# Kernel optimization log

Hardware: AMD Instinct MI355X
Metric: run time of the kernel (lower is better)

Reference implementation:

```python
import jax, jax.numpy as jnp
import numpy as np

N_NODES = 50000
IN_FEATS, H_FEATS, OUT_FEATS = 128, 128, 40
N_EDGES = 800000


def gcn_conv(x, src, dst, deg_inv_sqrt, W, b):
    # PyG GCNConv (eval): h = x @ W; msg = norm * h[src]; out = scatter_add(msg -> dst) + b
    h = x @ W  # [N, F_out]
    norm = deg_inv_sqrt[src] * deg_inv_sqrt[dst]  # [E+N] (self-loops included)
    msg = h[src] * norm[:, None]
    out = jax.ops.segment_sum(msg, dst, num_segments=x.shape[0])
    return out + b


def setup_inputs() -> dict:
    key = jax.random.key(0)
    k1, k2, k3, k4 = jax.random.split(key, 4)
    x = jax.random.normal(k1, (N_NODES, IN_FEATS), dtype=jnp.float32)
    edge_index = jax.random.randint(k2, (2, N_EDGES), 0, N_NODES, dtype=jnp.int64)
    # Glorot-ish init for weights, zeros for bias (PyG default)
    W1 = jax.random.normal(k3, (IN_FEATS, H_FEATS), dtype=jnp.float32) / np.sqrt(IN_FEATS)
    b1 = jnp.zeros((H_FEATS,), dtype=jnp.float32)
    W2 = jax.random.normal(k4, (H_FEATS, OUT_FEATS), dtype=jnp.float32) / np.sqrt(H_FEATS)
    b2 = jnp.zeros((OUT_FEATS,), dtype=jnp.float32)
    return {"x": x, "edge_index": edge_index, "W1": W1, "b1": b1, "W2": W2, "b2": b2}


def reference(x, edge_index, W1, b1, W2, b2):
    n = x.shape[0]
    loop = jnp.arange(n, dtype=edge_index.dtype)
    src = jnp.concatenate([edge_index[0], loop])  # add self-loops
    dst = jnp.concatenate([edge_index[1], loop])
    # symmetric normalization: deg over destinations (incl. self-loops)
    deg = jnp.zeros((n,), dtype=x.dtype).at[dst].add(1.0)
    deg_inv_sqrt = jnp.where(deg > 0, jax.lax.rsqrt(deg), 0.0)
    # dropout(p=0.6) is identity in eval mode
    h = jax.nn.relu(gcn_conv(x, src, dst, deg_inv_sqrt, W1, b1))
    out = gcn_conv(h, src, dst, deg_inv_sqrt, W2, b2)
    return out
```

## Files before the change

### kernel.cpp

```cpp
#include <hip/hip_runtime.h>
#include <hip/hip_fp16.h>

#define THREADS 256
#define EPB 2048


__global__ __launch_bounds__(256) void k_hist(const int* __restrict__ dst,
                                              int* __restrict__ Hmat,
                                              int e, int nbuck, int nbpad) {
    __shared__ int h[256];
    const int t = threadIdx.x;
    h[t] = 0;
    __syncthreads();
    const int base = blockIdx.x * EPB;
#pragma unroll
    for (int k = 0; k < 8; ++k) {
        int i = base + k * 256 + t;
        if (i < e) atomicAdd(&h[dst[i] >> 8], 1);
    }
    __syncthreads();
    if (t < nbuck) Hmat[t * nbpad + blockIdx.x] = h[t];
}

__global__ __launch_bounds__(256) void k_bscan(const int* __restrict__ Hmat,
                                               int* __restrict__ Off,
                                               int* __restrict__ btot,
                                               int nb, int nbpad) {
    __shared__ int s[256];
    const int b = blockIdx.x, t = threadIdx.x;
    const int* H = Hmat + b * nbpad;
    const int v0 = (2 * t     < nb) ? H[2 * t]     : 0;
    const int v1 = (2 * t + 1 < nb) ? H[2 * t + 1] : 0;
    const int p = v0 + v1;
    s[t] = p;
    __syncthreads();
    for (int off = 1; off < 256; off <<= 1) {
        int w = (t >= off) ? s[t - off] : 0;
        __syncthreads();
        s[t] += w;
        __syncthreads();
    }
    const int excl = s[t] - p;
    int* O = Off + b * nbpad;
    if (2 * t     < nb) O[2 * t]     = excl;
    if (2 * t + 1 < nb) O[2 * t + 1] = excl + v0;
    if (t == 255) btot[b] = s[255];
}

__global__ __launch_bounds__(256) void k_base(const int* __restrict__ btot,
                                              int* __restrict__ bbase,
                                              int* __restrict__ rowptr,
                                              int nbuck, int n, int e) {
    __shared__ int s[256];
    const int t = threadIdx.x;
    const int v = (t < nbuck) ? btot[t] : 0;
    s[t] = v;
    __syncthreads();
    for (int off = 1; off < 256; off <<= 1) {
        int w = (t >= off) ? s[t - off] : 0;
        __syncthreads();
        s[t] += w;
        __syncthreads();
    }
    if (t < nbuck) bbase[t] = s[t] - v;
    if (t == 0) { bbase[nbuck] = e; rowptr[n] = e; }
}

__global__ __launch_bounds__(256) void k_scat(const int* __restrict__ src,
                                              const int* __restrict__ dst,
                                              const int* __restrict__ Off,
                                              const int* __restrict__ bbase,
                                              int2* __restrict__ sorted,
                                              int e, int nbpad) {
    __shared__ int h[256];
    const int t = threadIdx.x;
    h[t] = 0;
    __syncthreads();
    const int base = blockIdx.x * EPB;
#pragma unroll
    for (int k = 0; k < 8; ++k) {
        int i = base + k * 256 + t;
        if (i < e) {
            const int d = dst[i];
            const int b = d >> 8;
            const int r = atomicAdd(&h[b], 1);
            const int pos = bbase[b] + Off[b * nbpad + blockIdx.x] + r;
            sorted[pos] = make_int2(src[i], d);
        }
    }
}

__global__ __launch_bounds__(256) void k_bsort(const int2* __restrict__ sorted,
                                               const int* __restrict__ bbase,
                                               int* __restrict__ csr_src,
                                               int* __restrict__ rowptr,
                                               float* __restrict__ dinv, int n) {
    __shared__ int cnt[256];
    __shared__ int s[256];
    __shared__ int fil[256];
    const int b = blockIdx.x, t = threadIdx.x;
    const int lo = bbase[b], hi = bbase[b + 1];
    cnt[t] = 0;
    __syncthreads();
    for (int p = lo + t; p < hi; p += 256) atomicAdd(&cnt[sorted[p].y & 255], 1);
    __syncthreads();
    const int c = cnt[t];
    s[t] = c;
    __syncthreads();
    for (int off = 1; off < 256; off <<= 1) {
        int w = (t >= off) ? s[t - off] : 0;
        __syncthreads();
        s[t] += w;
        __syncthreads();
    }
    const int excl = s[t] - c;
    const int node = b * 256 + t;
    if (node < n) {
        rowptr[node] = lo + excl;
        dinv[node] = rsqrtf((float)(c + 1));
    }
    fil[t] = lo + excl;
    __syncthreads();
    for (int p = lo + t; p < hi; p += 256) {
        const int2 pr = sorted[p];
        const int pos = atomicAdd(&fil[pr.y & 255], 1);
        csr_src[pos] = pr.x;
    }
}

__global__ __launch_bounds__(256) void k_gemm1(const float* __restrict__ x,
                                               const float* __restrict__ W,
                                               const float* __restrict__ dinv,
                                               __half2* __restrict__ g, int n) {
    __shared__ float Wl[64 * 128];
    __shared__ float xl[64 * 64];
    const int t  = threadIdx.x;
    const int cg = t & 31;
    const int rg = t >> 5;
    const int base = blockIdx.x * 64;

    float acc[8][4];
#pragma unroll
    for (int i = 0; i < 8; ++i)
#pragma unroll
        for (int j = 0; j < 4; ++j) acc[i][j] = 0.0f;

    for (int ph = 0; ph < 2; ++ph) {
        __syncthreads();
        {
            const float4* Wg = (const float4*)(W + ph * 64 * 128);
            float4* Ws = (float4*)Wl;
#pragma unroll
            for (int i = 0; i < 8; ++i) Ws[t + 256 * i] = Wg[t + 256 * i];
        }
#pragma unroll
        for (int i = 0; i < 4; ++i) {
            const int idx = t + 256 * i;
            const int r = idx >> 4, c4 = idx & 15;
            const int row = base + r;
            float4 v = make_float4(0.f, 0.f, 0.f, 0.f);
            if (row < n) v = *(const float4*)(x + (size_t)row * 128 + ph * 64 + c4 * 4);
            *(float4*)(xl + r * 64 + c4 * 4) = v;
        }
        __syncthreads();

        for (int k4 = 0; k4 < 16; ++k4) {
            float wv[4][4];
#pragma unroll
            for (int kk = 0; kk < 4; ++kk) {
                const float4 w4 = *(const float4*)(Wl + (k4 * 4 + kk) * 128 + cg * 4);
                wv[kk][0] = w4.x; wv[kk][1] = w4.y; wv[kk][2] = w4.z; wv[kk][3] = w4.w;
            }
#pragma unroll
            for (int i = 0; i < 8; ++i) {
                const float4 x4 = *(const float4*)(xl + (rg * 8 + i) * 64 + k4 * 4);
                const float xs[4] = {x4.x, x4.y, x4.z, x4.w};
#pragma unroll
                for (int kk = 0; kk < 4; ++kk)
#pragma unroll
                    for (int j = 0; j < 4; ++j)
                        acc[i][j] = fmaf(xs[kk], wv[kk][j], acc[i][j]);
            }
        }
    }

#pragma unroll
    for (int i = 0; i < 8; ++i) {
        const int row = base + rg * 8 + i;
        if (row < n) {
            const float dv = dinv[row];
            union { __half2 h[2]; uint2 u; } pk;
            pk.h[0] = __floats2half2_rn(acc[i][0] * dv, acc[i][1] * dv);
            pk.h[1] = __floats2half2_rn(acc[i][2] * dv, acc[i][3] * dv);
            *(uint2*)(g + (size_t)row * 64 + cg * 2) = pk.u;
        }
    }
}

__global__ __launch_bounds__(256) void k_gather1(const __half2* __restrict__ g,
                                                 const int* __restrict__ rowptr,
                                                 const int* __restrict__ csr_src,
                                                 const float* __restrict__ dinv,
                                                 const float* __restrict__ b1,
                                                 float* __restrict__ out1, int n) {
    const int wave = threadIdx.x >> 6;
    const int lane = threadIdx.x & 63;
    const int d = blockIdx.x * 4 + wave;
    if (d >= n) return;
    const int beg = rowptr[d], end = rowptr[d + 1];
    float ax = 0.f, ay = 0.f, bx = 0.f, by = 0.f;
    int p = beg;
    for (; p + 4 <= end; p += 4) {
        const int s0 = csr_src[p],     s1 = csr_src[p + 1];
        const int s2 = csr_src[p + 2], s3 = csr_src[p + 3];
        const __half2 v0 = g[(size_t)s0 * 64 + lane];
        const __half2 v1 = g[(size_t)s1 * 64 + lane];
        const __half2 v2 = g[(size_t)s2 * 64 + lane];
        const __half2 v3 = g[(size_t)s3 * 64 + lane];
        const float2 f0 = __half22float2(v0), f1 = __half22float2(v1);
        const float2 f2 = __half22float2(v2), f3 = __half22float2(v3);
        ax += f0.x + f2.x; ay += f0.y + f2.y;
        bx += f1.x + f3.x; by += f1.y + f3.y;
    }
    for (; p < end; ++p) {
        const int s0 = csr_src[p];
        const float2 f0 = __half22float2(g[(size_t)s0 * 64 + lane]);
        ax += f0.x; ay += f0.y;
    }
    const float2 fs = __half22float2(g[(size_t)d * 64 + lane]);
    ax += bx + fs.x;
    ay += by + fs.y;
    const float dd = dinv[d];
    const float2 bb = *(const float2*)(b1 + lane * 2);
    float2 r;
    r.x = fmaf(dd, ax, bb.x);
    r.y = fmaf(dd, ay, bb.y);
    *(float2*)(out1 + (size_t)d * 128 + lane * 2) = r;
}

__global__ __launch_bounds__(256) void k_gemm2(const float* __restrict__ h1,
                                               const float* __restrict__ W,
                                               const float* __restrict__ dinv,
                                               __half2* __restrict__ g, int n) {
    __shared__ float Wl[64 * 64];
    __shared__ float xl[64 * 64];
    const int t  = threadIdx.x;
    const int cg = t & 15;
    const int rg = t >> 4;
    const int base = blockIdx.x * 64;

    float acc[4][4];
#pragma unroll
    for (int i = 0; i < 4; ++i)
#pragma unroll
        for (int j = 0; j < 4; ++j) acc[i][j] = 0.0f;

    for (int ph = 0; ph < 2; ++ph) {
        __syncthreads();
#pragma unroll
        for (int i = 0; i < 16; ++i) {
            const int idx = t + 256 * i;
            const int r = idx >> 6, c = idx & 63;
            Wl[idx] = (c < 40) ? W[(ph * 64 + r) * 40 + c] : 0.0f;
        }
#pragma unroll
        for (int i = 0; i < 4; ++i) {
            const int idx = t + 256 * i;
            const int r = idx >> 4, c4 = idx & 15;
            const int row = base + r;
            float4 v = make_float4(0.f, 0.f, 0.f, 0.f);
            if (row < n) {
                v = *(const float4*)(h1 + (size_t)row * 128 + ph * 64 + c4 * 4);
                v.x = fmaxf(v.x, 0.f); v.y = fmaxf(v.y, 0.f);
                v.z = fmaxf(v.z, 0.f); v.w = fmaxf(v.w, 0.f);
            }
            *(float4*)(xl + r * 64 + c4 * 4) = v;
        }
        __syncthreads();

        for (int k4 = 0; k4 < 16; ++k4) {
            float wv[4][4];
#pragma unroll
            for (int kk = 0; kk < 4; ++kk) {
                const float4 w4 = *(const float4*)(Wl + (k4 * 4 + kk) * 64 + cg * 4);
                wv[kk][0] = w4.x; wv[kk][1] = w4.y; wv[kk][2] = w4.z; wv[kk][3] = w4.w;
            }
#pragma unroll
            for (int i = 0; i < 4; ++i) {
                const float4 x4 = *(const float4*)(xl + (rg * 4 + i) * 64 + k4 * 4);
                const float xs[4] = {x4.x, x4.y, x4.z, x4.w};
#pragma unroll
                for (int kk = 0; kk < 4; ++kk)
#pragma unroll
                    for (int j = 0; j < 4; ++j)
                        acc[i][j] = fmaf(xs[kk], wv[kk][j], acc[i][j]);
            }
        }
    }

    if (cg < 10) {
#pragma unroll
        for (int i = 0; i < 4; ++i) {
            const int row = base + rg * 4 + i;
            if (row < n) {
                const float dv = dinv[row];
                union { __half2 h[2]; uint2 u; } pk;
                pk.h[0] = __floats2half2_rn(acc[i][0] * dv, acc[i][1] * dv);
                pk.h[1] = __floats2half2_rn(acc[i][2] * dv, acc[i][3] * dv);
                *(uint2*)(g + (size_t)row * 20 + cg * 2) = pk.u;
            }
        }
    }
}

__global__ __launch_bounds__(256) void k_gather2(const __half2* __restrict__ g,
                                                 const int* __restrict__ rowptr,
                                                 const int* __restrict__ csr_src,
                                                 const float* __restrict__ dinv,
                                                 const float* __restrict__ b2,
                                                 float* __restrict__ out, int n) {
    const int wave = threadIdx.x >> 6;
    const int lane = threadIdx.x & 63;
    const int d = blockIdx.x * 4 + wave;
    if (d >= n) return;
    const int f  = lane & 31;
    const int eg = lane >> 5;
    const int fc = (f < 20) ? f : 19;
    const int beg = rowptr[d], end = rowptr[d + 1];
    float ax = 0.f, ay = 0.f;
    int p = beg + eg;
    for (; p + 2 < end; p += 4) {
        const int s0 = csr_src[p], s1 = csr_src[p + 2];
        const __half2 v0 = g[(size_t)s0 * 20 + fc];
        const __half2 v1 = g[(size_t)s1 * 20 + fc];
        const float2 f0 = __half22float2(v0), f1 = __half22float2(v1);
        ax += f0.x + f1.x;
        ay += f0.y + f1.y;
    }
    for (; p < end; p += 2) {
        const int s0 = csr_src[p];
        const float2 f0 = __half22float2(g[(size_t)s0 * 20 + fc]);
        ax += f0.x; ay += f0.y;
    }
    ax += __shfl_xor(ax, 32);
    ay += __shfl_xor(ay, 32);
    if (eg == 0 && f < 20) {
        const float2 fs = __half22float2(g[(size_t)d * 20 + f]);
        ax += fs.x; ay += fs.y;
        const float dd = dinv[d];
        const float2 bb = *(const float2*)(b2 + f * 2);
        float2 r;
        r.x = fmaf(dd, ax, bb.x);
        r.y = fmaf(dd, ay, bb.y);
        *(float2*)(out + (size_t)d * 40 + f * 2) = r;
    }
}

extern "C" void kernel_launch(void* const* d_in, const int* in_sizes, int n_in,
                              void* d_out, int out_size, void* d_ws, size_t ws_size,
                              hipStream_t stream) {
    const float* x  = (const float*)d_in[0];
    const int*   ei = (const int*)d_in[1];
    const float* W1 = (const float*)d_in[2];
    const float* b1 = (const float*)d_in[3];
    const float* W2 = (const float*)d_in[4];
    const float* b2 = (const float*)d_in[5];
    float* out = (float*)d_out;

    const int n = in_sizes[0] / 128;
    const int e = in_sizes[1] / 2;
    const int* src = ei;
    const int* dst = ei + e;

    const int n_pad = ((n + 63) / 64) * 64;
    const int e_pad = ((e + 63) / 64) * 64;
    const int NB    = (e + EPB - 1) / EPB;
    const int nbuck = (n + 255) >> 8;
    const int nbpad = ((NB + 63) / 64) * 64;

    float*   ws      = (float*)d_ws;
    float*   dinv    = ws;
    int*     rowptr  = (int*)(ws + n_pad);
    int*     csr_src = rowptr + n_pad + 64;
    __half2* g1      = (__half2*)(csr_src + e_pad);
    float*   out1    = (float*)((int*)g1 + (size_t)n_pad * 64);
    int2*    sorted  = (int2*)g1;
    int*     Hmat    = (int*)g1 + (size_t)e_pad * 2;
    int*     Off     = Hmat + nbuck * nbpad;
    int*     btot    = Off + nbuck * nbpad;
    int*     bbase   = btot + ((nbuck + 63) / 64) * 64;
    __half2* g2      = g1;

    const int nb_rows = (n + 63) / 64;
    const int nb_g    = (n + 3) / 4;

    k_hist <<<NB,    256, 0, stream>>>(dst, Hmat, e, nbuck, nbpad);
    k_bscan<<<nbuck, 256, 0, stream>>>(Hmat, Off, btot, NB, nbpad);
    k_base <<<1,     256, 0, stream>>>(btot, bbase, rowptr, nbuck, n, e);
    k_scat <<<NB,    256, 0, stream>>>(src, dst, Off, bbase, sorted, e, nbpad);
    k_bsort<<<nbuck, 256, 0, stream>>>(sorted, bbase, csr_src, rowptr, dinv, n);

    k_gemm1  <<<nb_rows, 256, 0, stream>>>(x, W1, dinv, g1, n);
    k_gather1<<<nb_g, 256, 0, stream>>>(g1, rowptr, csr_src, dinv, b1, out1, n);

    k_gemm2  <<<nb_rows, 256, 0, stream>>>(out1, W2, dinv, g2, n);
    k_gather2<<<nb_g, 256, 0, stream>>>(g2, rowptr, csr_src, dinv, b2, out, n);
}
```

Measured before the change: 158.1 us.

## Use fp16 MFMA for both GEMMs and store hidden layer in fp16 with fused ReLU

Both dense projections now convert inputs and weights to fp16 in LDS and use 16x16x32 MFMA instructions in place of scalar FMA tiles. The first gather applies ReLU and writes the hidden features as half2, so the second GEMM reads half the bytes and skips its own ReLU. The aim is to cut GEMM compute time and the hidden-layer memory traffic, at the cost of fp16 rounding of x and the hidden activations, plus narrower scalar half stores in the GEMM epilogues.

```diff
diff --git a/kernel.cpp b/kernel.cpp
--- a/kernel.cpp
+++ b/kernel.cpp
@@ -3,6 +3,10 @@
 
 #define THREADS 256
 #define EPB 2048
+#define LDK 136
+
+using f16x8 = __attribute__((ext_vector_type(8))) _Float16;
+using f32x4 = __attribute__((ext_vector_type(4))) float;
 
 
 __global__ __launch_bounds__(256) void k_hist(const int* __restrict__ dst,
@@ -131,68 +135,57 @@
 __global__ __launch_bounds__(256) void k_gemm1(const float* __restrict__ x,
                                                const float* __restrict__ W,
                                                const float* __restrict__ dinv,
-                                               __half2* __restrict__ g, int n) {
-    __shared__ float Wl[64 * 128];
-    __shared__ float xl[64 * 64];
+                                               __half* __restrict__ g, int n) {
+    __shared__ _Float16 Wt[128 * LDK];
+    __shared__ _Float16 xl[64 * LDK];
     const int t  = threadIdx.x;
-    const int cg = t & 31;
-    const int rg = t >> 5;
+    const int wv = t >> 6;
+    const int l  = t & 63;
     const int base = blockIdx.x * 64;
 
-    float acc[8][4];
-#pragma unroll
-    for (int i = 0; i < 8; ++i)
-#pragma unroll
-        for (int j = 0; j < 4; ++j) acc[i][j] = 0.0f;
-
-    for (int ph = 0; ph < 2; ++ph) {
-        __syncthreads();
-        {
-            const float4* Wg = (const float4*)(W + ph * 64 * 128);
-            float4* Ws = (float4*)Wl;
-#pragma unroll
-            for (int i = 0; i < 8; ++i) Ws[t + 256 * i] = Wg[t + 256 * i];
-        }
-#pragma unroll
-        for (int i = 0; i < 4; ++i) {
-            const int idx = t + 256 * i;
-            const int r = idx >> 4, c4 = idx & 15;
-            const int row = base + r;
-            float4 v = make_float4(0.f, 0.f, 0.f, 0.f);
-            if (row < n) v = *(const float4*)(x + (size_t)row * 128 + ph * 64 + c4 * 4);
-            *(float4*)(xl + r * 64 + c4 * 4) = v;
-        }
-        __syncthreads();
-
-        for (int k4 = 0; k4 < 16; ++k4) {
-            float wv[4][4];
-#pragma unroll
-            for (int kk = 0; kk < 4; ++kk) {
-                const float4 w4 = *(const float4*)(Wl + (k4 * 4 + kk) * 128 + cg * 4);
-                wv[kk][0] = w4.x; wv[kk][1] = w4.y; wv[kk][2] = w4.z; wv[kk][3] = w4.w;
-            }
-#pragma unroll
-            for (int i = 0; i < 8; ++i) {
-                const float4 x4 = *(const float4*)(xl + (rg * 8 + i) * 64 + k4 * 4);
-                const float xs[4] = {x4.x, x4.y, x4.z, x4.w};
-#pragma unroll
-                for (int kk = 0; kk < 4; ++kk)
-#pragma unroll
-                    for (int j = 0; j < 4; ++j)
-                        acc[i][j] = fmaf(xs[kk], wv[kk][j], acc[i][j]);
-            }
-        }
-    }
-
+#pragma unroll
+    for (int i = 0; i < 64; ++i) {
+        const int idx = t + 256 * i;
+        const int nn = idx & 127, kk = idx >> 7;
+        Wt[nn * LDK + kk] = (_Float16)W[kk * 128 + nn];
+    }
 #pragma unroll
     for (int i = 0; i < 8; ++i) {
-        const int row = base + rg * 8 + i;
+        const int idx = t + 256 * i;
+        const int r = idx >> 5, c4 = idx & 31;
+        const int row = base + r;
+        float4 v = make_float4(0.f, 0.f, 0.f, 0.f);
+        if (row < n) v = *(const float4*)(x + (size_t)row * 128 + c4 * 4);
+        _Float16* p = xl + r * LDK + c4 * 4;
+        p[0] = (_Float16)v.x; p[1] = (_Float16)v.y;
+        p[2] = (_Float16)v.z; p[3] = (_Float16)v.w;
+    }
+    __syncthreads();
+
+    f32x4 acc[8];
+#pragma unroll
+    for (int i = 0; i < 8; ++i) acc[i] = (f32x4){0.f, 0.f, 0.f, 0.f};
+
+    const int arow = wv * 16 + (l & 15);
+    const int koff = (l >> 4) * 8;
+#pragma unroll
+    for (int kb = 0; kb < 4; ++kb) {
+        const f16x8 a = *(const f16x8*)(xl + arow * LDK + kb * 32 + koff);
+#pragma unroll
+        for (int nt = 0; nt < 8; ++nt) {
+            const f16x8 b = *(const f16x8*)(Wt + (nt * 16 + (l & 15)) * LDK + kb * 32 + koff);
+            acc[nt] = __builtin_amdgcn_mfma_f32_16x16x32_f16(a, b, acc[nt], 0, 0, 0);
+        }
+    }
+
+#pragma unroll
+    for (int i = 0; i < 4; ++i) {
+        const int row = base + wv * 16 + (l >> 4) * 4 + i;
         if (row < n) {
             const float dv = dinv[row];
-            union { __half2 h[2]; uint2 u; } pk;
-            pk.h[0] = __floats2half2_rn(acc[i][0] * dv, acc[i][1] * dv);
-            pk.h[1] = __floats2half2_rn(acc[i][2] * dv, acc[i][3] * dv);
-            *(uint2*)(g + (size_t)row * 64 + cg * 2) = pk.u;
+#pragma unroll
+            for (int nt = 0; nt < 8; ++nt)
+                g[(size_t)row * 128 + nt * 16 + (l & 15)] = __float2half(acc[nt][i] * dv);
         }
     }
 }
@@ -202,7 +195,7 @@
                                                  const int* __restrict__ csr_src,
                                                  const float* __restrict__ dinv,
                                                  const float* __restrict__ b1,
-                                                 float* __restrict__ out1, int n) {
+                                                 __half2* __restrict__ out1, int n) {
     const int wave = threadIdx.x >> 6;
     const int lane = threadIdx.x & 63;
     const int d = blockIdx.x * 4 + wave;
@@ -232,82 +225,65 @@
     ay += by + fs.y;
     const float dd = dinv[d];
     const float2 bb = *(const float2*)(b1 + lane * 2);
-    float2 r;
-    r.x = fmaf(dd, ax, bb.x);
-    r.y = fmaf(dd, ay, bb.y);
-    *(float2*)(out1 + (size_t)d * 128 + lane * 2) = r;
-}
-
-__global__ __launch_bounds__(256) void k_gemm2(const float* __restrict__ h1,
+    const float rx = fmaxf(fmaf(dd, ax, bb.x), 0.f);
+    const float ry = fmaxf(fmaf(dd, ay, bb.y), 0.f);
+    out1[(size_t)d * 64 + lane] = __floats2half2_rn(rx, ry);
+}
+
+__global__ __launch_bounds__(256) void k_gemm2(const __half* __restrict__ h1,
                                                const float* __restrict__ W,
                                                const float* __restrict__ dinv,
-                                               __half2* __restrict__ g, int n) {
-    __shared__ float Wl[64 * 64];
-    __shared__ float xl[64 * 64];
+                                               __half* __restrict__ g, int n) {
+    __shared__ _Float16 Wt[48 * LDK];
+    __shared__ _Float16 xl[64 * LDK];
     const int t  = threadIdx.x;
-    const int cg = t & 15;
-    const int rg = t >> 4;
+    const int wv = t >> 6;
+    const int l  = t & 63;
     const int base = blockIdx.x * 64;
 
-    float acc[4][4];
-#pragma unroll
-    for (int i = 0; i < 4; ++i)
-#pragma unroll
-        for (int j = 0; j < 4; ++j) acc[i][j] = 0.0f;
-
-    for (int ph = 0; ph < 2; ++ph) {
-        __syncthreads();
-#pragma unroll
-        for (int i = 0; i < 16; ++i) {
-            const int idx = t + 256 * i;
-            const int r = idx >> 6, c = idx & 63;
-            Wl[idx] = (c < 40) ? W[(ph * 64 + r) * 40 + c] : 0.0f;
-        }
-#pragma unroll
-        for (int i = 0; i < 4; ++i) {
-            const int idx = t + 256 * i;
-            const int r = idx >> 4, c4 = idx & 15;
-            const int row = base + r;
-            float4 v = make_float4(0.f, 0.f, 0.f, 0.f);
-            if (row < n) {
-                v = *(const float4*)(h1 + (size_t)row * 128 + ph * 64 + c4 * 4);
-                v.x = fmaxf(v.x, 0.f); v.y = fmaxf(v.y, 0.f);
-                v.z = fmaxf(v.z, 0.f); v.w = fmaxf(v.w, 0.f);
-            }
-            *(float4*)(xl + r * 64 + c4 * 4) = v;
-        }
-        __syncthreads();
-
-        for (int k4 = 0; k4 < 16; ++k4) {
-            float wv[4][4];
-#pragma unroll
-            for (int kk = 0; kk < 4; ++kk) {
-                const float4 w4 = *(const float4*)(Wl + (k4 * 4 + kk) * 64 + cg * 4);
-                wv[kk][0] = w4.x; wv[kk][1] = w4.y; wv[kk][2] = w4.z; wv[kk][3] = w4.w;
-            }
-#pragma unroll
-            for (int i = 0; i < 4; ++i) {
-                const float4 x4 = *(const float4*)(xl + (rg * 4 + i) * 64 + k4 * 4);
-                const float xs[4] = {x4.x, x4.y, x4.z, x4.w};
-#pragma unroll
-                for (int kk = 0; kk < 4; ++kk)
-#pragma unroll
-                    for (int j = 0; j < 4; ++j)
-                        acc[i][j] = fmaf(xs[kk], wv[kk][j], acc[i][j]);
-            }
-        }
-    }
-
-    if (cg < 10) {
-#pragma unroll
-        for (int i = 0; i < 4; ++i) {
-            const int row = base + rg * 4 + i;
-            if (row < n) {
-                const float dv = dinv[row];
-                union { __half2 h[2]; uint2 u; } pk;
-                pk.h[0] = __floats2half2_rn(acc[i][0] * dv, acc[i][1] * dv);
-                pk.h[1] = __floats2half2_rn(acc[i][2] * dv, acc[i][3] * dv);
-                *(uint2*)(g + (size_t)row * 20 + cg * 2) = pk.u;
+#pragma unroll
+    for (int i = 0; i < 24; ++i) {
+        const int idx = t + 256 * i;
+        const int nn = idx % 48, kk = idx / 48;
+        Wt[nn * LDK + kk] = (nn < 40) ? (_Float16)W[kk * 40 + nn] : (_Float16)0.f;
+    }
+#pragma unroll
+    for (int i = 0; i < 4; ++i) {
+        const int idx = t + 256 * i;
+        const int r = idx >> 4, c8 = idx & 15;
+        const int row = base + r;
+        uint4 v = make_uint4(0u, 0u, 0u, 0u);
+        if (row < n) v = *(const uint4*)(h1 + (size_t)row * 128 + c8 * 8);
+        *(uint4*)(xl + r * LDK + c8 * 8) = v;
+    }
+    __syncthreads();
+
+    f32x4 acc[3];
+#pragma unroll
+    for (int i = 0; i < 3; ++i) acc[i] = (f32x4){0.f, 0.f, 0.f, 0.f};
+
+    const int arow = wv * 16 + (l & 15);
+    const int koff = (l >> 4) * 8;
+#pragma unroll
+    for (int kb = 0; kb < 4; ++kb) {
+        const f16x8 a = *(const f16x8*)(xl + arow * LDK + kb * 32 + koff);
+#pragma unroll
+        for (int nt = 0; nt < 3; ++nt) {
+            const f16x8 b = *(const f16x8*)(Wt + (nt * 16 + (l & 15)) * LDK + kb * 32 + koff);
+            acc[nt] = __builtin_amdgcn_mfma_f32_16x16x32_f16(a, b, acc[nt], 0, 0, 0);
+        }
+    }
+
+#pragma unroll
+    for (int i = 0; i < 4; ++i) {
+        const int row = base + wv * 16 + (l >> 4) * 4 + i;
+        if (row < n) {
+            const float dv = dinv[row];
+#pragma unroll
+            for (int nt = 0; nt < 3; ++nt) {
+                const int col = nt * 16 + (l & 15);
+                if (col < 40)
+                    g[(size_t)row * 40 + col] = __float2half(acc[nt][i] * dv);
             }
         }
     }
@@ -383,7 +359,7 @@
     int*     rowptr  = (int*)(ws + n_pad);
     int*     csr_src = rowptr + n_pad + 64;
     __half2* g1      = (__half2*)(csr_src + e_pad);
-    float*   out1    = (float*)((int*)g1 + (size_t)n_pad * 64);
+    __half*  out1h   = (__half*)(g1 + (size_t)n_pad * 64);
     int2*    sorted  = (int2*)g1;
     int*     Hmat    = (int*)g1 + (size_t)e_pad * 2;
     int*     Off     = Hmat + nbuck * nbpad;
@@ -400,9 +376,9 @@
     k_scat <<<NB,    256, 0, stream>>>(src, dst, Off, bbase, sorted, e, nbpad);
     k_bsort<<<nbuck, 256, 0, stream>>>(sorted, bbase, csr_src, rowptr, dinv, n);
 
-    k_gemm1  <<<nb_rows, 256, 0, stream>>>(x, W1, dinv, g1, n);
-    k_gather1<<<nb_g, 256, 0, stream>>>(g1, rowptr, csr_src, dinv, b1, out1, n);
-
-    k_gemm2  <<<nb_rows, 256, 0, stream>>>(out1, W2, dinv, g2, n);
+    k_gemm1  <<<nb_rows, 256, 0, stream>>>(x, W1, dinv, (__half*)g1, n);
+    k_gather1<<<nb_g, 256, 0, stream>>>(g1, rowptr, csr_src, dinv, b1, (__half2*)out1h, n);
+
+    k_gemm2  <<<nb_rows, 256, 0, stream>>>(out1h, W2, dinv, (__half*)g2, n);
     k_gather2<<<nb_g, 256, 0, stream>>>(g2, rowptr, csr_src, dinv, b2, out, n);
 }
```

After: 136.9 us. -13.4%, faster.
